# Kernel optimization log

Measured on AMD Instinct MI355X. Metric: run time of the kernel, lower is better.

## Reference

```python
import jax, jax.numpy as jnp
import numpy as np

NUM_GRAPHS = 512  # static number of segments (graphs in the batch)
EPS = 1e-05


def setup_inputs() -> dict:
    key = jax.random.key(0)
    k1, k2 = jax.random.split(key)
    N, C = 500000, 128
    x = jax.random.normal(k1, (N, C), dtype=jnp.float32)
    batch = jnp.sort(jax.random.randint(k2, (N,), 0, NUM_GRAPHS)).astype(jnp.int64)
    weight = jnp.ones((C,), dtype=jnp.float32)
    bias = jnp.zeros((C,), dtype=jnp.float32)
    return {"x": x, "batch": batch, "weight": weight, "bias": bias}


def reference(x, batch, weight, bias):
    # Per-graph mean/var over nodes (dim=0 within each graph), per channel.
    seg = batch.astype(jnp.int32)
    counts = jax.ops.segment_sum(jnp.ones((x.shape[0],), x.dtype), seg,
                                 num_segments=NUM_GRAPHS)  # [B]
    counts = jnp.maximum(counts, 1.0)[:, None]             # guard empty graphs
    sums = jax.ops.segment_sum(x, seg, num_segments=NUM_GRAPHS)          # [B, C]
    sqsums = jax.ops.segment_sum(x * x, seg, num_segments=NUM_GRAPHS)    # [B, C]
    mean = sums / counts                                   # [B, C]
    var = sqsums / counts - mean * mean                    # biased (unbiased=False)
    inv_std = jax.lax.rsqrt(var + EPS)
    out = (x - mean[seg]) * inv_std[seg]                   # gather per node
    return out * weight + bias
```

## Files before the change

### kernel.cpp

```cpp
#include <hip/hip_runtime.h>

#define NUM_GRAPHS 512
#define EPS 1e-5f
#define CHN 128
#define CHN4 32
#define RPB 256

typedef float f32x4 __attribute__((ext_vector_type(4)));

__device__ __forceinline__ int lower_bound_i(const int* __restrict__ b, int n, int val) {
    int l = 0, r = n;
    while (l < r) {
        int m = (l + r) >> 1;
        if (b[m] < val) l = m + 1; else r = m;
    }
    return l;
}

__global__ __launch_bounds__(128) void gln_offsets(
    const int* __restrict__ batch, int* __restrict__ seg_off, int N)
{
    int s = blockIdx.x * 128 + threadIdx.x;
    if (s < NUM_GRAPHS)       seg_off[s] = lower_bound_i(batch, N, s);
    else if (s == NUM_GRAPHS) seg_off[s] = N;
}

__global__ __launch_bounds__(1024) void gln_stats(
    const float* __restrict__ x,
    const int* __restrict__ seg_off,
    const float* __restrict__ weight,
    const float* __restrict__ bias,
    float* __restrict__ ws_stats)
{
    const int s   = blockIdx.x;
    const int tid = threadIdx.x;
    const int q   = tid & 31;
    const int g   = tid >> 5;

    const int lo = seg_off[s];
    const int hi = seg_off[s + 1];

    const float4* __restrict__ x4 = (const float4*)x;

    float4 sum = make_float4(0.f, 0.f, 0.f, 0.f);
    float4 sq  = make_float4(0.f, 0.f, 0.f, 0.f);
    for (int r = lo + g; r < hi; r += 32) {
        float4 v = x4[(size_t)r * CHN4 + q];
        sum.x += v.x; sum.y += v.y; sum.z += v.z; sum.w += v.w;
        sq.x  += v.x * v.x; sq.y += v.y * v.y; sq.z += v.z * v.z; sq.w += v.w * v.w;
    }

    __shared__ float4 s_sum[1024];
    __shared__ float4 s_sq[1024];
    s_sum[tid] = sum; s_sq[tid] = sq;
    __syncthreads();

    #pragma unroll
    for (int off = 512; off >= 32; off >>= 1) {
        if (tid < off) {
            float4 a = s_sum[tid], b = s_sum[tid + off];
            a.x += b.x; a.y += b.y; a.z += b.z; a.w += b.w;
            s_sum[tid] = a;
            float4 c = s_sq[tid], d = s_sq[tid + off];
            c.x += d.x; c.y += d.y; c.z += d.z; c.w += d.w;
            s_sq[tid] = c;
        }
        __syncthreads();
    }

    if (tid < CHN) {
        float sum_c = ((const float*)s_sum)[tid];
        float sq_c  = ((const float*)s_sq)[tid];
        float inv_cnt = 1.f / fmaxf((float)(hi - lo), 1.f);
        float mean    = sum_c * inv_cnt;
        float inv_std = rsqrtf(sq_c * inv_cnt - mean * mean + EPS);
        float scale = inv_std * weight[tid];
        float shift = bias[tid] - mean * scale;
        ws_stats[(size_t)s * 256 + tid]       = scale;
        ws_stats[(size_t)s * 256 + 128 + tid] = shift;
    }
}

__global__ __launch_bounds__(256) void gln_normalize(
    const float* __restrict__ x,
    const int* __restrict__ batch,
    const int* __restrict__ seg_off,
    const float* __restrict__ ws_stats,
    float* __restrict__ out, int N)
{
    const int tid = threadIdx.x;
    const int q   = tid & 31;
    const int g   = tid >> 5;

    const int row0 = blockIdx.x * RPB + g;
    const int rend = min(blockIdx.x * RPB + RPB, N);
    if (row0 >= rend) return;

    int seg = batch[row0];
    int hi  = seg_off[seg + 1];

    const float4* __restrict__ st4 = (const float4*)ws_stats;
    float4 sc = st4[(size_t)seg * 64 + q];
    float4 sh = st4[(size_t)seg * 64 + 32 + q];

    const f32x4* __restrict__ x4 = (const f32x4*)x;
    f32x4* __restrict__ o4       = (f32x4*)out;

    for (int r = row0; r < rend; r += 8) {
        while (r >= hi) {
            ++seg;
            hi = seg_off[seg + 1];
            sc = st4[(size_t)seg * 64 + q];
            sh = st4[(size_t)seg * 64 + 32 + q];
        }
        const f32x4 v = __builtin_nontemporal_load(x4 + ((size_t)r * CHN4 + q));
        f32x4 o;
        o.x = fmaf(v.x, sc.x, sh.x);
        o.y = fmaf(v.y, sc.y, sh.y);
        o.z = fmaf(v.z, sc.z, sh.z);
        o.w = fmaf(v.w, sc.w, sh.w);
        __builtin_nontemporal_store(o, o4 + ((size_t)r * CHN4 + q));
    }
}

extern "C" void kernel_launch(void* const* d_in, const int* in_sizes, int n_in,
                              void* d_out, int out_size, void* d_ws, size_t ws_size,
                              hipStream_t stream) {
    const float* x      = (const float*)d_in[0];
    const int*   batch  = (const int*)d_in[1];
    const float* weight = (const float*)d_in[2];
    const float* bias   = (const float*)d_in[3];
    float*       out    = (float*)d_out;
    const int N = in_sizes[0] / CHN;

    int*   seg_off  = (int*)d_ws;
    float* ws_stats = (float*)((char*)d_ws + 4096);

    gln_offsets<<<(NUM_GRAPHS + 1 + 127) / 128, 128, 0, stream>>>(batch, seg_off, N);
    gln_stats<<<NUM_GRAPHS, 1024, 0, stream>>>(x, seg_off, weight, bias, ws_stats);
    gln_normalize<<<(N + RPB - 1) / RPB, 256, 0, stream>>>(x, batch, seg_off, ws_stats, out, N);
}
```

Before: 474.2 us.

## Fuse offsets, stats and normalize into one per-segment kernel

Replaces the three kernels with one block per graph segment. Each block finds its own row range via a wave-parallel ballot lower bound, reduces sums and squared sums, keeps scale and shift in shared memory, then normalizes the same rows. This removes two launches and the workspace round trip, and lets the second read of each segment hit cache. In exchange the normalize phase is limited to 512 blocks, and the nontemporal hints are dropped.

```diff
diff --git a/kernel.cpp b/kernel.cpp
--- a/kernel.cpp
+++ b/kernel.cpp
@@ -4,41 +4,42 @@
 #define EPS 1e-5f
 #define CHN 128
 #define CHN4 32
-#define RPB 256
+#define TPB 1024
 
 typedef float f32x4 __attribute__((ext_vector_type(4)));
 
-__device__ __forceinline__ int lower_bound_i(const int* __restrict__ b, int n, int val) {
-    int l = 0, r = n;
-    while (l < r) {
-        int m = (l + r) >> 1;
-        if (b[m] < val) l = m + 1; else r = m;
+__device__ __forceinline__ int wave_lower_bound(const int* __restrict__ b, int n, int val) {
+    int lo = 0, hi = n;
+    const int lane = threadIdx.x & 63;
+    while (hi > lo) {
+        const int len  = hi - lo;
+        const int step = (len + 63) >> 6;
+        const int pos  = lo + lane * step;
+        const bool p   = (pos < hi) && (b[pos] < val);
+        const unsigned long long m = __ballot(p);
+        if (m == 0ULL) return lo;
+        const int k = 63 - __clzll(m);
+        lo = lo + k * step + 1;
+        const int nhi = lo - 1 + step;
+        hi = (nhi < hi) ? nhi : hi;
     }
-    return l;
+    return lo;
 }
 
-__global__ __launch_bounds__(128) void gln_offsets(
-    const int* __restrict__ batch, int* __restrict__ seg_off, int N)
-{
-    int s = blockIdx.x * 128 + threadIdx.x;
-    if (s < NUM_GRAPHS)       seg_off[s] = lower_bound_i(batch, N, s);
-    else if (s == NUM_GRAPHS) seg_off[s] = N;
-}
-
-__global__ __launch_bounds__(1024) void gln_stats(
+__global__ __launch_bounds__(TPB) void gln_fused(
     const float* __restrict__ x,
-    const int* __restrict__ seg_off,
+    const int* __restrict__ batch,
     const float* __restrict__ weight,
     const float* __restrict__ bias,
-    float* __restrict__ ws_stats)
+    float* __restrict__ out, int N)
 {
     const int s   = blockIdx.x;
     const int tid = threadIdx.x;
     const int q   = tid & 31;
     const int g   = tid >> 5;
 
-    const int lo = seg_off[s];
-    const int hi = seg_off[s + 1];
+    const int lo = wave_lower_bound(batch, N, s);
+    const int hi = wave_lower_bound(batch, N, s + 1);
 
     const float4* __restrict__ x4 = (const float4*)x;
 
@@ -50,8 +51,8 @@
         sq.x  += v.x * v.x; sq.y += v.y * v.y; sq.z += v.z * v.z; sq.w += v.w * v.w;
     }
 
-    __shared__ float4 s_sum[1024];
-    __shared__ float4 s_sq[1024];
+    __shared__ float4 s_sum[TPB];
+    __shared__ float4 s_sq[TPB];
     s_sum[tid] = sum; s_sq[tid] = sq;
     __syncthreads();
 
@@ -68,6 +69,8 @@
         __syncthreads();
     }
 
+    __shared__ float s_scale[CHN];
+    __shared__ float s_shift[CHN];
     if (tid < CHN) {
         float sum_c = ((const float*)s_sum)[tid];
         float sq_c  = ((const float*)s_sq)[tid];
@@ -75,45 +78,18 @@
         float mean    = sum_c * inv_cnt;
         float inv_std = rsqrtf(sq_c * inv_cnt - mean * mean + EPS);
         float scale = inv_std * weight[tid];
-        float shift = bias[tid] - mean * scale;
-        ws_stats[(size_t)s * 256 + tid]       = scale;
-        ws_stats[(size_t)s * 256 + 128 + tid] = shift;
+        s_scale[tid] = scale;
+        s_shift[tid] = bias[tid] - mean * scale;
     }
-}
+    __syncthreads();
 
-__global__ __launch_bounds__(256) void gln_normalize(
-    const float* __restrict__ x,
-    const int* __restrict__ batch,
-    const int* __restrict__ seg_off,
-    const float* __restrict__ ws_stats,
-    float* __restrict__ out, int N)
-{
-    const int tid = threadIdx.x;
-    const int q   = tid & 31;
-    const int g   = tid >> 5;
+    const float4 sc = ((const float4*)s_scale)[q];
+    const float4 sh = ((const float4*)s_shift)[q];
 
-    const int row0 = blockIdx.x * RPB + g;
-    const int rend = min(blockIdx.x * RPB + RPB, N);
-    if (row0 >= rend) return;
-
-    int seg = batch[row0];
-    int hi  = seg_off[seg + 1];
-
-    const float4* __restrict__ st4 = (const float4*)ws_stats;
-    float4 sc = st4[(size_t)seg * 64 + q];
-    float4 sh = st4[(size_t)seg * 64 + 32 + q];
-
-    const f32x4* __restrict__ x4 = (const f32x4*)x;
-    f32x4* __restrict__ o4       = (f32x4*)out;
-
-    for (int r = row0; r < rend; r += 8) {
-        while (r >= hi) {
-            ++seg;
-            hi = seg_off[seg + 1];
-            sc = st4[(size_t)seg * 64 + q];
-            sh = st4[(size_t)seg * 64 + 32 + q];
-        }
-        const f32x4 v = __builtin_nontemporal_load(x4 + ((size_t)r * CHN4 + q));
+    const f32x4* __restrict__ xx4 = (const f32x4*)x;
+    f32x4* __restrict__ o4        = (f32x4*)out;
+    for (int r = lo + g; r < hi; r += 32) {
+        const f32x4 v = xx4[(size_t)r * CHN4 + q];
         f32x4 o;
         o.x = fmaf(v.x, sc.x, sh.x);
         o.y = fmaf(v.y, sc.y, sh.y);
@@ -133,10 +109,5 @@
     float*       out    = (float*)d_out;
     const int N = in_sizes[0] / CHN;
 
-    int*   seg_off  = (int*)d_ws;
-    float* ws_stats = (float*)((char*)d_ws + 4096);
-
-    gln_offsets<<<(NUM_GRAPHS + 1 + 127) / 128, 128, 0, stream>>>(batch, seg_off, N);
-    gln_stats<<<NUM_GRAPHS, 1024, 0, stream>>>(x, seg_off, weight, bias, ws_stats);
-    gln_normalize<<<(N + RPB - 1) / RPB, 256, 0, stream>>>(x, batch, seg_off, ws_stats, out, N);
+    gln_fused<<<NUM_GRAPHS, TPB, 0, stream>>>(x, batch, weight, bias, out, N);
 }
```

Result: faster. 462.9 us (-2.4%).
